# Optimization experiments

Measured on AMD Instinct MI355X. Metric: run time of the kernel, lower is better.

Reference implementation:

```python
import jax, jax.numpy as jnp
import numpy as np

B, N, C = 8, 4096, 512
K = 512   # key_channels
V = 512   # value_channels (must equal in_channels for reprojection to typecheck)
H = 8     # head_count


def setup_inputs() -> dict:
    key = jax.random.key(0)
    ks = jax.random.split(key, 10)
    s = 1.0 / np.sqrt(C)
    return {
        "input_": jax.random.normal(ks[0], (B, N, C), jnp.float32),
        "y": jax.random.normal(ks[1], (B, N, C), jnp.float32),
        "Wk": jax.random.uniform(ks[2], (C, K), jnp.float32, -s, s),
        "bk": jax.random.uniform(ks[3], (K,), jnp.float32, -s, s),
        "Wq": jax.random.uniform(ks[4], (C, K), jnp.float32, -s, s),
        "bq": jax.random.uniform(ks[5], (K,), jnp.float32, -s, s),
        "Wv": jax.random.uniform(ks[6], (C, K), jnp.float32, -s, s),
        "bv": jax.random.uniform(ks[7], (K,), jnp.float32, -s, s),
        "Wr": jax.random.uniform(ks[8], (C, K), jnp.float32, -s, s),
        "br": jax.random.uniform(ks[9], (K,), jnp.float32, -s, s),
    }


def reference(input_, y, Wk, bk, Wq, bq, Wv, bv, Wr, br):
    hk = K // H  # head key channels
    hv = V // H  # head value channels
    # projections -> [B, N, H, h]
    keys = ((input_ + y) @ Wk + bk).reshape(B, N, H, hk)
    queries = (y @ Wq + bq).reshape(B, N, H, hk)
    values = (input_ @ Wv + bv).reshape(B, N, H, hv)
    # key softmax over tokens N; query softmax over head channels hk
    keys = jax.nn.softmax(keys, axis=1)
    queries = jax.nn.softmax(queries, axis=3)
    # context[b,h,k,v] = sum_n key[b,n,h,k] * value[b,n,h,v]
    context = jnp.einsum('bnhk,bnhv->bhkv', keys, values)
    # attended[b,n,h,v] = sum_k context[b,h,k,v] * query[b,n,h,k]
    attended = jnp.einsum('bhkv,bnhk->bnhv', context, queries)
    aggregated = attended.reshape(B, N, V)  # concat heads over value channels
    return aggregated @ Wr + br
```

## Files before the change

### kernel.cpp

```cpp
#include <hip/hip_runtime.h>
#include <hip/hip_bf16.h>
#include <stdint.h>


typedef __attribute__((ext_vector_type(8))) short short8;
typedef __attribute__((ext_vector_type(4))) float f32x4;
typedef __attribute__((ext_vector_type(4))) unsigned short us4;

__device__ __forceinline__ unsigned short f2bf(float f) {
  union { float f; unsigned u; } v; v.f = f;
  unsigned r = v.u + 0x7FFFu + ((v.u >> 16) & 1u);
  return (unsigned short)(r >> 16);
}
__device__ __forceinline__ float bf2f(unsigned short u) {
  union { unsigned u; float f; } v; v.u = ((unsigned)u) << 16;
  return v.f;
}
__device__ __forceinline__ ushort2 pk2(float a, float b) {
  __hip_bfloat162 h = __float22bfloat162_rn(float2{a, b});
  return *reinterpret_cast<ushort2*>(&h);
}
__device__ __forceinline__ void gload16(const void* g, void* l) {
  __builtin_amdgcn_global_load_lds(
      (const __attribute__((address_space(1))) void*)g,
      (__attribute__((address_space(3))) void*)l, 16, 0, 0);
}

__global__ void prep_w(const float* __restrict__ Wk, const float* __restrict__ Wq,
                       const float* __restrict__ Wv, const float* __restrict__ Wr,
                       unsigned short* __restrict__ Wt) {
  __shared__ float tile[64][65];
  const int t = threadIdx.x;
  const int bx = blockIdx.x, by = blockIdx.y, w = blockIdx.z;
  const float* W = (w == 0) ? Wk : (w == 1) ? Wq : (w == 2) ? Wv : Wr;
  unsigned short* O = Wt + (size_t)w * 512 * 512;
#pragma unroll
  for (int p = 0; p < 16; ++p) {
    int idx = p * 256 + t; int r = idx >> 6, c = idx & 63;
    tile[r][c] = W[(size_t)(by * 64 + r) * 512 + bx * 64 + c];
  }
  __syncthreads();
#pragma unroll
  for (int p = 0; p < 16; ++p) {
    int idx = p * 256 + t; int r = idx >> 6, c = idx & 63;
    O[(size_t)(bx * 64 + r) * 512 + by * 64 + c] = f2bf(tile[c][r]);
  }
}

__global__ __launch_bounds__(256) void prep_xy(const float* __restrict__ x, const float* __restrict__ y,
                        unsigned short* __restrict__ xb, unsigned short* __restrict__ yb,
                        unsigned short* __restrict__ xyb) {
  const size_t i = ((size_t)blockIdx.x * 256 + threadIdx.x) * 16;
  float4 a[4], b[4];
#pragma unroll
  for (int q = 0; q < 4; ++q) a[q] = *(const float4*)(x + i + q * 4);
#pragma unroll
  for (int q = 0; q < 4; ++q) b[q] = *(const float4*)(y + i + q * 4);
#pragma unroll
  for (int h = 0; h < 2; ++h) {
    float4 a0 = a[2 * h], a1 = a[2 * h + 1], b0 = b[2 * h], b1 = b[2 * h + 1];
    short8 vx, vy, vs;
    ushort2 p;
    p = pk2(a0.x, a0.y); vx[0] = (short)p.x; vx[1] = (short)p.y;
    p = pk2(a0.z, a0.w); vx[2] = (short)p.x; vx[3] = (short)p.y;
    p = pk2(a1.x, a1.y); vx[4] = (short)p.x; vx[5] = (short)p.y;
    p = pk2(a1.z, a1.w); vx[6] = (short)p.x; vx[7] = (short)p.y;
    p = pk2(b0.x, b0.y); vy[0] = (short)p.x; vy[1] = (short)p.y;
    p = pk2(b0.z, b0.w); vy[2] = (short)p.x; vy[3] = (short)p.y;
    p = pk2(b1.x, b1.y); vy[4] = (short)p.x; vy[5] = (short)p.y;
    p = pk2(b1.z, b1.w); vy[6] = (short)p.x; vy[7] = (short)p.y;
    p = pk2(a0.x + b0.x, a0.y + b0.y); vs[0] = (short)p.x; vs[1] = (short)p.y;
    p = pk2(a0.z + b0.z, a0.w + b0.w); vs[2] = (short)p.x; vs[3] = (short)p.y;
    p = pk2(a1.x + b1.x, a1.y + b1.y); vs[4] = (short)p.x; vs[5] = (short)p.y;
    p = pk2(a1.z + b1.z, a1.w + b1.w); vs[6] = (short)p.x; vs[7] = (short)p.y;
    *(short8*)(xb + i + h * 8) = vx;
    *(short8*)(yb + i + h * 8) = vy;
    *(short8*)(xyb + i + h * 8) = vs;
  }
}

template <int MODE>
__global__ __launch_bounds__(256) void gemm_bf16(const unsigned short* __restrict__ A,
                          const unsigned short* __restrict__ Bmat,
                          const float* __restrict__ bias, void* __restrict__ OutV,
                          float* __restrict__ S) {
  __shared__ __align__(16) unsigned short As[2][128][64];
  __shared__ __align__(16) unsigned short Bs[2][128][64];
  const int t = threadIdx.x, l = t & 63, w = t >> 6;
  const int lr = l & 15, lg = l >> 4;
  const int wr = w >> 1, wc = w & 1;
  const int bid = blockIdx.x;
  const int swz = (bid & 7) * 128 + (bid >> 3);
  const int tn = swz & 3, tm = swz >> 2;

  const unsigned short* Bbase = (MODE == 3) ? (Bmat + (size_t)(tm >> 5) * 262144) : Bmat;
  const int r0 = w * 8 + (l >> 3);
  const int su = ((l & 7) ^ (l >> 3)) * 8;
  const unsigned short* Ag = A + (size_t)(tm * 128 + r0) * 512 + su;
  const unsigned short* Bg = Bbase + (size_t)(tn * 128 + r0) * 512 + su;

  f32x4 acc[4][4] = {};

#define PSTAGE(buf, kt)                                                        \
  {                                                                            \
    _Pragma("unroll") for (int i = 0; i < 4; ++i) {                            \
      gload16(Ag + (size_t)i * 32 * 512 + (kt) * 64, &As[buf][i * 32 + w * 8][0]); \
      gload16(Bg + (size_t)i * 32 * 512 + (kt) * 64, &Bs[buf][i * 32 + w * 8][0]); \
    }                                                                          \
  }

  PSTAGE(0, 0)
  PSTAGE(1, 1)
  for (int kt = 0; kt < 8; ++kt) {
    const int cur = kt & 1;
    if (kt < 7) { asm volatile("s_waitcnt vmcnt(8)" ::: "memory"); }
    else        { asm volatile("s_waitcnt vmcnt(0)" ::: "memory"); }
    __builtin_amdgcn_s_barrier();
    asm volatile("" ::: "memory");
    __builtin_amdgcn_s_setprio(1);
#pragma unroll
    for (int kk = 0; kk < 2; ++kk) {
      short8 af[4], bf[4];
#pragma unroll
      for (int m = 0; m < 4; ++m)
        af[m] = *(const short8*)&As[cur][wr * 64 + m * 16 + lr][((kk * 4 + lg) ^ (lr & 7)) * 8];
#pragma unroll
      for (int n = 0; n < 4; ++n)
        bf[n] = *(const short8*)&Bs[cur][wc * 64 + n * 16 + lr][((kk * 4 + lg) ^ (lr & 7)) * 8];
#pragma unroll
      for (int m = 0; m < 4; ++m)
#pragma unroll
        for (int n = 0; n < 4; ++n)
          acc[m][n] = __builtin_amdgcn_mfma_f32_16x16x32_bf16(af[m], bf[n], acc[m][n], 0, 0, 0);
    }
    __builtin_amdgcn_s_setprio(0);
    asm volatile("" ::: "memory");
    __builtin_amdgcn_s_barrier();
    asm volatile("" ::: "memory");
    if (kt < 6) PSTAGE(cur, kt + 2)
  }
#undef PSTAGE

  const int c_base = tn * 128 + wc * 64;
  const int r_base = tm * 128 + wr * 64;
  float bv_[4];
#pragma unroll
  for (int n = 0; n < 4; ++n) bv_[n] = bias[c_base + n * 16 + lr];

  if (MODE == 1) {
    unsigned short* Out = (unsigned short*)OutV;
#pragma unroll
    for (int m = 0; m < 4; ++m) {
#pragma unroll
      for (int j = 0; j < 4; ++j) {
        float a0 = acc[m][0][j] + bv_[0], a1 = acc[m][1][j] + bv_[1];
        float a2 = acc[m][2][j] + bv_[2], a3 = acc[m][3][j] + bv_[3];
        float mx = fmaxf(fmaxf(a0, a1), fmaxf(a2, a3));
#pragma unroll
        for (int o = 1; o < 16; o <<= 1) mx = fmaxf(mx, __shfl_xor(mx, o));
        float e0 = __expf(a0 - mx), e1 = __expf(a1 - mx);
        float e2 = __expf(a2 - mx), e3 = __expf(a3 - mx);
        float s = e0 + e1 + e2 + e3;
#pragma unroll
        for (int o = 1; o < 16; o <<= 1) s += __shfl_xor(s, o);
        const float rs = 1.0f / s;
        const int row = r_base + m * 16 + lg * 4 + j;
        Out[(size_t)row * 512 + c_base + 0 * 16 + lr] = f2bf(e0 * rs);
        Out[(size_t)row * 512 + c_base + 1 * 16 + lr] = f2bf(e1 * rs);
        Out[(size_t)row * 512 + c_base + 2 * 16 + lr] = f2bf(e2 * rs);
        Out[(size_t)row * 512 + c_base + 3 * 16 + lr] = f2bf(e3 * rs);
      }
    }
  } else if (MODE == 3) {
    float* Out = (float*)OutV;
#pragma unroll
    for (int n = 0; n < 4; ++n) {
      const int col = c_base + n * 16 + lr;
#pragma unroll
      for (int m = 0; m < 4; ++m) {
        const int row = r_base + m * 16 + lg * 4;
#pragma unroll
        for (int j = 0; j < 4; ++j)
          Out[(size_t)(row + j) * 512 + col] = acc[m][n][j] + bv_[n];
      }
    }
  } else if (MODE == 0) {
    unsigned short* Out = (unsigned short*)OutV;
    const int b = (tm * 128) >> 12;
#pragma unroll
    for (int n = 0; n < 4; ++n) {
      const int col = c_base + n * 16 + lr;
      float srow = 0.f;
#pragma unroll
      for (int m = 0; m < 4; ++m) {
        const int row = r_base + m * 16 + lg * 4;
        const int nl = row & 4095;
        us4 v;
#pragma unroll
        for (int j = 0; j < 4; ++j) {
          float f = __expf(acc[m][n][j] + bv_[n]);
          srow += f;
          v[j] = f2bf(f);
        }
        *(us4*)&Out[((size_t)(b * 512 + col)) * 4096 + nl] = v;
      }
      srow += __shfl_xor(srow, 16);
      srow += __shfl_xor(srow, 32);
      if (lg == 0) atomicAdd(&S[b * 512 + col], srow);
    }
  } else {
    unsigned short* Out = (unsigned short*)OutV;
    const int b = (tm * 128) >> 12;
#pragma unroll
    for (int n = 0; n < 4; ++n) {
      const int col = c_base + n * 16 + lr;
#pragma unroll
      for (int m = 0; m < 4; ++m) {
        const int row = r_base + m * 16 + lg * 4;
        const int nl = row & 4095;
        us4 v;
#pragma unroll
        for (int j = 0; j < 4; ++j) v[j] = f2bf(acc[m][n][j] + bv_[n]);
        *(us4*)&Out[((size_t)(b * 512 + col)) * 4096 + nl] = v;
      }
    }
  }
}

__global__ void context_partial(const unsigned short* __restrict__ KeT,
                                const unsigned short* __restrict__ VT,
                                float* __restrict__ cp) {
  const int t = threadIdx.x, l = t & 63, w = t >> 6;
  const int lr = l & 15, lg = l >> 4;
  const int ch = blockIdx.x, h = blockIdx.y, b = blockIdx.z;
  const unsigned short* Kp = KeT + ((size_t)b * 512 + h * 64) * 4096;
  const unsigned short* Vp = VT + ((size_t)b * 512 + h * 64) * 4096;
  const int tok_w = ch * 1024 + w * 256;
  f32x4 acc[4][4] = {};
  for (int s = 0; s < 8; ++s) {
    const int tok = tok_w + s * 32 + lg * 8;
    short8 a[4], kf[4];
#pragma unroll
    for (int m = 0; m < 4; ++m) a[m] = *(const short8*)&Vp[(size_t)(m * 16 + lr) * 4096 + tok];
#pragma unroll
    for (int n = 0; n < 4; ++n) kf[n] = *(const short8*)&Kp[(size_t)(n * 16 + lr) * 4096 + tok];
#pragma unroll
    for (int m = 0; m < 4; ++m)
#pragma unroll
      for (int n = 0; n < 4; ++n)
        acc[m][n] = __builtin_amdgcn_mfma_f32_16x16x32_bf16(a[m], kf[n], acc[m][n], 0, 0, 0);
  }
  __shared__ float red[4][64][64];
#pragma unroll
  for (int m = 0; m < 4; ++m)
#pragma unroll
    for (int n = 0; n < 4; ++n)
#pragma unroll
      for (int j = 0; j < 4; ++j)
        red[w][m * 16 + lg * 4 + j][n * 16 + lr] = acc[m][n][j];
  __syncthreads();
  const int blk = (b * 8 + h) * 4 + ch;
  float* o = cp + (size_t)blk * 4096;
  for (int i = 0; i < 16; ++i) {
    int e = i * 256 + t;
    int v = e >> 6, k = e & 63;
    o[e] = red[0][v][k] + red[1][v][k] + red[2][v][k] + red[3][v][k];
  }
}

__global__ void ctx_reduce(const float* __restrict__ cp, const float* __restrict__ S,
                           unsigned short* __restrict__ ctxN) {
  const int bh = blockIdx.x, t = threadIdx.x;
  const float* p = cp + (size_t)bh * 4 * 4096;
  for (int i = 0; i < 16; ++i) {
    int e = i * 256 + t;
    float vsum = p[e] + p[4096 + e] + p[8192 + e] + p[12288 + e];
    int v = e >> 6, k = e & 63;
    ctxN[(size_t)bh * 4096 + k * 64 + v] = f2bf(vsum / S[bh * 64 + k]);
  }
}

__global__ void ctx_mm(const unsigned short* __restrict__ ctxN, const unsigned short* __restrict__ Wrt,
                       unsigned short* __restrict__ MT) {
  const int t = threadIdx.x, l = t & 63, w = t >> 6;
  const int lr = l & 15, lg = l >> 4;
  const int h = blockIdx.x, b = blockIdx.y;
  const unsigned short* Ap = ctxN + (size_t)(b * 8 + h) * 4096;
  f32x4 acc[4][8] = {};
  const int c0 = w * 128;
#pragma unroll
  for (int kk = 0; kk < 2; ++kk) {
    const int vb = kk * 32 + lg * 8;
    short8 a[4], bfr[8];
#pragma unroll
    for (int m = 0; m < 4; ++m) a[m] = *(const short8*)&Ap[(m * 16 + lr) * 64 + vb];
#pragma unroll
    for (int n = 0; n < 8; ++n) bfr[n] = *(const short8*)&Wrt[(size_t)(c0 + n * 16 + lr) * 512 + h * 64 + vb];
#pragma unroll
    for (int m = 0; m < 4; ++m)
#pragma unroll
      for (int n = 0; n < 8; ++n)
        acc[m][n] = __builtin_amdgcn_mfma_f32_16x16x32_bf16(a[m], bfr[n], acc[m][n], 0, 0, 0);
  }
#pragma unroll
  for (int n = 0; n < 8; ++n) {
    const int c = c0 + n * 16 + lr;
#pragma unroll
    for (int m = 0; m < 4; ++m) {
      const int k = m * 16 + lg * 4;
      us4 v;
#pragma unroll
      for (int j = 0; j < 4; ++j) v[j] = f2bf(acc[m][n][j]);
      *(us4*)&MT[((size_t)b * 512 + c) * 512 + h * 64 + k] = v;
    }
  }
}

extern "C" void kernel_launch(void* const* d_in, const int* in_sizes, int n_in,
                              void* d_out, int out_size, void* d_ws, size_t ws_size,
                              hipStream_t stream) {
  (void)in_sizes; (void)n_in; (void)out_size;
  const float* x  = (const float*)d_in[0];
  const float* y  = (const float*)d_in[1];
  const float* Wk = (const float*)d_in[2];
  const float* bk = (const float*)d_in[3];
  const float* Wq = (const float*)d_in[4];
  const float* bq = (const float*)d_in[5];
  const float* Wv = (const float*)d_in[6];
  const float* bv = (const float*)d_in[7];
  const float* Wr = (const float*)d_in[8];
  const float* br = (const float*)d_in[9];
  float* out = (float*)d_out;

  char* ws = (char*)d_ws;
  unsigned short* Wt   = (unsigned short*)(ws + 0);
  unsigned short* xb   = (unsigned short*)(ws + 2097152);
  unsigned short* yb   = (unsigned short*)(ws + 35651584);
  unsigned short* xyb  = (unsigned short*)(ws + 69206016);
  unsigned short* KeT  = (unsigned short*)(ws + 102760448);
  unsigned short* VT   = (unsigned short*)(ws + 136314880);
  float* S             = (float*)(ws + 169869312);
  float* cp            = (float*)(ws + 169885696);
  unsigned short* ctxN = (unsigned short*)(ws + 174080000);
  unsigned short* MT   = (unsigned short*)(ws + 174604288);
  unsigned short* Qp   = xyb;

  prep_w<<<dim3(8, 8, 4), 256, 0, stream>>>(Wk, Wq, Wv, Wr, Wt);
  prep_xy<<<4096, 256, 0, stream>>>(x, y, xb, yb, xyb);
  hipMemsetAsync(S, 0, 512 * 8 * sizeof(float), stream);
  gemm_bf16<0><<<1024, 256, 0, stream>>>(xyb, Wt, bk, KeT, S);
  gemm_bf16<2><<<1024, 256, 0, stream>>>(xb, Wt + 2 * 262144, bv, VT, nullptr);
  gemm_bf16<1><<<1024, 256, 0, stream>>>(yb, Wt + 262144, bq, Qp, nullptr);
  context_partial<<<dim3(4, 8, 8), 256, 0, stream>>>(KeT, VT, cp);
  ctx_reduce<<<64, 256, 0, stream>>>(cp, S, ctxN);
  ctx_mm<<<dim3(8, 8), 256, 0, stream>>>(ctxN, Wt + 3 * 262144, MT);
  gemm_bf16<3><<<1024, 256, 0, stream>>>(Qp, MT, br, out, nullptr);
}
```

Measured before the change: 217.5 us.

## Fuse context reduction into ctx matmul and restructure prep_xy access pattern

Merges the ctx_reduce kernel into the context-times-Wr matmul: each block now sums the four partial contexts, normalizes by S, and stages the bf16 context in LDS before running the MFMA. The grid grows from 64 to 256 blocks, with each block covering a quarter of the output channels. This removes one launch and the ctxN round trip through global memory, at the cost of repeating the reduction in the four blocks of each head. Separately, prep_xy moves from 16 elements per thread to 8, using fully coalesced float4 loads over twice as many blocks.

```diff
diff --git a/kernel.cpp b/kernel.cpp
--- a/kernel.cpp
+++ b/kernel.cpp
@@ -19,6 +19,11 @@
 __device__ __forceinline__ ushort2 pk2(float a, float b) {
   __hip_bfloat162 h = __float22bfloat162_rn(float2{a, b});
   return *reinterpret_cast<ushort2*>(&h);
+}
+__device__ __forceinline__ us4 cvt4(float4 a) {
+  ushort2 c0 = pk2(a.x, a.y), c1 = pk2(a.z, a.w);
+  us4 r; r[0] = c0.x; r[1] = c0.y; r[2] = c1.x; r[3] = c1.y;
+  return r;
 }
 __device__ __forceinline__ void gload16(const void* g, void* l) {
   __builtin_amdgcn_global_load_lds(
@@ -50,33 +55,21 @@
 __global__ __launch_bounds__(256) void prep_xy(const float* __restrict__ x, const float* __restrict__ y,
                         unsigned short* __restrict__ xb, unsigned short* __restrict__ yb,
                         unsigned short* __restrict__ xyb) {
-  const size_t i = ((size_t)blockIdx.x * 256 + threadIdx.x) * 16;
-  float4 a[4], b[4];
-#pragma unroll
-  for (int q = 0; q < 4; ++q) a[q] = *(const float4*)(x + i + q * 4);
-#pragma unroll
-  for (int q = 0; q < 4; ++q) b[q] = *(const float4*)(y + i + q * 4);
-#pragma unroll
-  for (int h = 0; h < 2; ++h) {
-    float4 a0 = a[2 * h], a1 = a[2 * h + 1], b0 = b[2 * h], b1 = b[2 * h + 1];
-    short8 vx, vy, vs;
-    ushort2 p;
-    p = pk2(a0.x, a0.y); vx[0] = (short)p.x; vx[1] = (short)p.y;
-    p = pk2(a0.z, a0.w); vx[2] = (short)p.x; vx[3] = (short)p.y;
-    p = pk2(a1.x, a1.y); vx[4] = (short)p.x; vx[5] = (short)p.y;
-    p = pk2(a1.z, a1.w); vx[6] = (short)p.x; vx[7] = (short)p.y;
-    p = pk2(b0.x, b0.y); vy[0] = (short)p.x; vy[1] = (short)p.y;
-    p = pk2(b0.z, b0.w); vy[2] = (short)p.x; vy[3] = (short)p.y;
-    p = pk2(b1.x, b1.y); vy[4] = (short)p.x; vy[5] = (short)p.y;
-    p = pk2(b1.z, b1.w); vy[6] = (short)p.x; vy[7] = (short)p.y;
-    p = pk2(a0.x + b0.x, a0.y + b0.y); vs[0] = (short)p.x; vs[1] = (short)p.y;
-    p = pk2(a0.z + b0.z, a0.w + b0.w); vs[2] = (short)p.x; vs[3] = (short)p.y;
-    p = pk2(a1.x + b1.x, a1.y + b1.y); vs[4] = (short)p.x; vs[5] = (short)p.y;
-    p = pk2(a1.z + b1.z, a1.w + b1.w); vs[6] = (short)p.x; vs[7] = (short)p.y;
-    *(short8*)(xb + i + h * 8) = vx;
-    *(short8*)(yb + i + h * 8) = vy;
-    *(short8*)(xyb + i + h * 8) = vs;
-  }
+  const size_t base = (size_t)blockIdx.x * 2048;
+  const int t = threadIdx.x;
+  const size_t i1 = base + t * 4, i2 = base + 1024 + t * 4;
+  float4 x1 = *(const float4*)(x + i1);
+  float4 x2 = *(const float4*)(x + i2);
+  float4 y1 = *(const float4*)(y + i1);
+  float4 y2 = *(const float4*)(y + i2);
+  float4 s1{x1.x + y1.x, x1.y + y1.y, x1.z + y1.z, x1.w + y1.w};
+  float4 s2{x2.x + y2.x, x2.y + y2.y, x2.z + y2.z, x2.w + y2.w};
+  *(us4*)(xb + i1) = cvt4(x1);
+  *(us4*)(xb + i2) = cvt4(x2);
+  *(us4*)(yb + i1) = cvt4(y1);
+  *(us4*)(yb + i2) = cvt4(y2);
+  *(us4*)(xyb + i1) = cvt4(s1);
+  *(us4*)(xyb + i2) = cvt4(s2);
 }
 
 template <int MODE>
@@ -268,50 +261,59 @@
   }
 }
 
-__global__ void ctx_reduce(const float* __restrict__ cp, const float* __restrict__ S,
-                           unsigned short* __restrict__ ctxN) {
-  const int bh = blockIdx.x, t = threadIdx.x;
-  const float* p = cp + (size_t)bh * 4 * 4096;
-  for (int i = 0; i < 16; ++i) {
-    int e = i * 256 + t;
-    float vsum = p[e] + p[4096 + e] + p[8192 + e] + p[12288 + e];
-    int v = e >> 6, k = e & 63;
-    ctxN[(size_t)bh * 4096 + k * 64 + v] = f2bf(vsum / S[bh * 64 + k]);
-  }
-}
-
-__global__ void ctx_mm(const unsigned short* __restrict__ ctxN, const unsigned short* __restrict__ Wrt,
-                       unsigned short* __restrict__ MT) {
+__global__ __launch_bounds__(256) void ctx_mm2(const float* __restrict__ cp,
+                      const float* __restrict__ S, const unsigned short* __restrict__ Wrt,
+                      unsigned short* __restrict__ MT) {
+  __shared__ __align__(16) unsigned short ctx_lds[64][72];
   const int t = threadIdx.x, l = t & 63, w = t >> 6;
   const int lr = l & 15, lg = l >> 4;
-  const int h = blockIdx.x, b = blockIdx.y;
-  const unsigned short* Ap = ctxN + (size_t)(b * 8 + h) * 4096;
-  f32x4 acc[4][8] = {};
-  const int c0 = w * 128;
+  const int cc = blockIdx.x, h = blockIdx.y, b = blockIdx.z;
+  const int bh = b * 8 + h;
+
+  const int k = t & 63, vg = t >> 6;
+  const float rs = 1.0f / S[bh * 64 + k];
+  const float* pb = cp + (size_t)bh * 4 * 4096 + k;
+#pragma unroll
+  for (int half = 0; half < 2; ++half) {
+    short8 pkv;
+#pragma unroll
+    for (int i = 0; i < 8; ++i) {
+      const int v = vg * 16 + half * 8 + i;
+      const size_t e = (size_t)v * 64;
+      float vsum = pb[e] + pb[4096 + e] + pb[8192 + e] + pb[12288 + e];
+      pkv[i] = (short)f2bf(vsum * rs);
+    }
+    *(short8*)&ctx_lds[k][vg * 16 + half * 8] = pkv;
+  }
+  __syncthreads();
+
+  const int c0 = cc * 128 + w * 32;
+  f32x4 acc[4][2] = {};
 #pragma unroll
   for (int kk = 0; kk < 2; ++kk) {
     const int vb = kk * 32 + lg * 8;
-    short8 a[4], bfr[8];
-#pragma unroll
-    for (int m = 0; m < 4; ++m) a[m] = *(const short8*)&Ap[(m * 16 + lr) * 64 + vb];
-#pragma unroll
-    for (int n = 0; n < 8; ++n) bfr[n] = *(const short8*)&Wrt[(size_t)(c0 + n * 16 + lr) * 512 + h * 64 + vb];
+    short8 a[4], bfr[2];
+#pragma unroll
+    for (int m = 0; m < 4; ++m) a[m] = *(const short8*)&ctx_lds[m * 16 + lr][vb];
+#pragma unroll
+    for (int n = 0; n < 2; ++n)
+      bfr[n] = *(const short8*)&Wrt[(size_t)(c0 + n * 16 + lr) * 512 + h * 64 + vb];
 #pragma unroll
     for (int m = 0; m < 4; ++m)
 #pragma unroll
-      for (int n = 0; n < 8; ++n)
+      for (int n = 0; n < 2; ++n)
         acc[m][n] = __builtin_amdgcn_mfma_f32_16x16x32_bf16(a[m], bfr[n], acc[m][n], 0, 0, 0);
   }
 #pragma unroll
-  for (int n = 0; n < 8; ++n) {
+  for (int n = 0; n < 2; ++n) {
     const int c = c0 + n * 16 + lr;
 #pragma unroll
     for (int m = 0; m < 4; ++m) {
-      const int k = m * 16 + lg * 4;
+      const int kq = m * 16 + lg * 4;
       us4 v;
 #pragma unroll
       for (int j = 0; j < 4; ++j) v[j] = f2bf(acc[m][n][j]);
-      *(us4*)&MT[((size_t)b * 512 + c) * 512 + h * 64 + k] = v;
+      *(us4*)&MT[((size_t)b * 512 + c) * 512 + h * 64 + kq] = v;
     }
   }
 }
@@ -319,7 +321,7 @@
 extern "C" void kernel_launch(void* const* d_in, const int* in_sizes, int n_in,
                               void* d_out, int out_size, void* d_ws, size_t ws_size,
                               hipStream_t stream) {
-  (void)in_sizes; (void)n_in; (void)out_size;
+  (void)in_sizes; (void)n_in; (void)out_size; (void)ws_size;
   const float* x  = (const float*)d_in[0];
   const float* y  = (const float*)d_in[1];
   const float* Wk = (const float*)d_in[2];
@@ -341,18 +343,16 @@
   unsigned short* VT   = (unsigned short*)(ws + 136314880);
   float* S             = (float*)(ws + 169869312);
   float* cp            = (float*)(ws + 169885696);
-  unsigned short* ctxN = (unsigned short*)(ws + 174080000);
-  unsigned short* MT   = (unsigned short*)(ws + 174604288);
+  unsigned short* MT   = (unsigned short*)(ws + 174080000);
   unsigned short* Qp   = xyb;
 
   prep_w<<<dim3(8, 8, 4), 256, 0, stream>>>(Wk, Wq, Wv, Wr, Wt);
-  prep_xy<<<4096, 256, 0, stream>>>(x, y, xb, yb, xyb);
+  prep_xy<<<8192, 256, 0, stream>>>(x, y, xb, yb, xyb);
   hipMemsetAsync(S, 0, 512 * 8 * sizeof(float), stream);
   gemm_bf16<0><<<1024, 256, 0, stream>>>(xyb, Wt, bk, KeT, S);
   gemm_bf16<2><<<1024, 256, 0, stream>>>(xb, Wt + 2 * 262144, bv, VT, nullptr);
   gemm_bf16<1><<<1024, 256, 0, stream>>>(yb, Wt + 262144, bq, Qp, nullptr);
   context_partial<<<dim3(4, 8, 8), 256, 0, stream>>>(KeT, VT, cp);
-  ctx_reduce<<<64, 256, 0, stream>>>(cp, S, ctxN);
-  ctx_mm<<<dim3(8, 8), 256, 0, stream>>>(ctxN, Wt + 3 * 262144, MT);
+  ctx_mm2<<<dim3(4, 8, 8), 256, 0, stream>>>(cp, S, Wt + 3 * 262144, MT);
   gemm_bf16<3><<<1024, 256, 0, stream>>>(Qp, MT, br, out, nullptr);
 }
```

Measured after the change: 187.7 us. 13.7% less time.
